# Optimization experiments

Hardware: AMD Instinct MI355X
Metric: run time of the kernel (lower is better)

## Reference

```python
import jax, jax.numpy as jnp
import numpy as np
import math

B, S, D, H, FF = 4, 1024, 1024, 16, 4096
DK = D // H
EPS = 1e-6


def _gelu(x):
    return 0.5 * x * (1 + jnp.tanh(math.sqrt(2 / math.pi) * (x + 0.044715 * x ** 3)))


def _layernorm(x, g, b):
    # torch LayerNorm clone: unbiased std, divide by (std + eps)
    mean = jnp.mean(x, axis=-1, keepdims=True)
    var = jnp.sum((x - mean) ** 2, axis=-1, keepdims=True) / (x.shape[-1] - 1)
    std = jnp.sqrt(var)
    return g * (x - mean) / (std + EPS) + b


def setup_inputs() -> dict:
    key = jax.random.key(0)
    ks = jax.random.split(key, 16)
    sc_d = 1.0 / math.sqrt(D)
    sc_ff = 1.0 / math.sqrt(FF)
    inp = {
        "query": jax.random.normal(ks[0], (B, S, D), jnp.float32),
        "key": jax.random.normal(ks[1], (B, S, D), jnp.float32),
        "value": jax.random.normal(ks[2], (B, S, D), jnp.float32),
        "mask": jnp.ones((B, S), jnp.int32),
        "Wq": jax.random.normal(ks[3], (D, D), jnp.float32) * sc_d,
        "bq": jnp.zeros((D,), jnp.float32),
        "Wk": jax.random.normal(ks[4], (D, D), jnp.float32) * sc_d,
        "bk": jnp.zeros((D,), jnp.float32),
        "Wv": jax.random.normal(ks[5], (D, D), jnp.float32) * sc_d,
        "bv": jnp.zeros((D,), jnp.float32),
        "Wo": jax.random.normal(ks[6], (D, D), jnp.float32) * sc_d,
        "bo": jnp.zeros((D,), jnp.float32),
        "W1": jax.random.normal(ks[7], (FF, D), jnp.float32) * sc_d,
        "b1": jnp.zeros((FF,), jnp.float32),
        "W2": jax.random.normal(ks[8], (D, FF), jnp.float32) * sc_ff,
        "b2": jnp.zeros((D,), jnp.float32),
        "g1": jnp.ones((D,), jnp.float32),
        "be1": jnp.zeros((D,), jnp.float32),
        "g2": jnp.ones((D,), jnp.float32),
        "be2": jnp.zeros((D,), jnp.float32),
    }
    return inp


def reference(query, key, value, mask, Wq, bq, Wk, bk, Wv, bv, Wo, bo,
              W1, b1, W2, b2, g1, be1, g2, be2):
    # self-attention: q = k = v = query (with_external=False)
    def proj(x, W, b):
        return (x @ W.T + b).reshape(B, S, H, DK).transpose(0, 2, 1, 3)  # [B,H,S,DK]

    q = proj(query, Wq, bq)
    k = proj(query, Wk, bk)
    v = proj(query, Wv, bv)
    scores = jnp.einsum("bhqd,bhkd->bhqk", q, k) / math.sqrt(DK)
    # 2D mask [B,S] broadcasts as [B,1,1,S] over key positions
    scores = jnp.where(mask[:, None, None, :] == 0, -1e9, scores)
    p = jax.nn.softmax(scores, axis=-1)
    attn = jnp.einsum("bhqk,bhkd->bhqd", p, v)
    attn = attn.transpose(0, 2, 1, 3).reshape(B, S, D)
    x = attn @ Wo.T + bo
    x = _layernorm(query + x, g1, be1)
    residual = x
    h1 = x @ W1.T + b1
    x2 = _gelu(h1 @ W2.T + b2)  # note: gelu applied AFTER fc2, per source
    return _layernorm(residual + x2, g2, be2)
```

## Files before the change

### kernel.cpp

```cpp
#include <hip/hip_runtime.h>
#include <hip/hip_bf16.h>
#include <math.h>

typedef __bf16 bf16;
typedef __bf16 bf16x8 __attribute__((ext_vector_type(8)));
typedef float floatx4 __attribute__((ext_vector_type(4)));

#define NT 4096
#define DMODEL 1024
#define NHEAD 16
#define DHEAD 64
#define FFDIM 4096

__device__ __forceinline__ void load_lds16(const void* g, void* l) {
    __builtin_amdgcn_global_load_lds(
        (const __attribute__((address_space(1))) void*)g,
        (__attribute__((address_space(3))) void*)l,
        16, 0, 0);
}

__device__ __forceinline__ unsigned short f2bf(float f) {
    bf16 h = (bf16)f;
    return __builtin_bit_cast(unsigned short, h);
}

__device__ __forceinline__ float gelu_f(float v) {
    return 0.5f * v * (1.0f + tanhf(0.7978845608028654f * (v + 0.044715f * v * v * v)));
}

__global__ __launch_bounds__(256) void cast_kernel(
    const float* __restrict__ q, const float* __restrict__ wq, const float* __restrict__ wk,
    const float* __restrict__ wv, const float* __restrict__ wo, const float* __restrict__ w1,
    const float* __restrict__ w2, const float* __restrict__ bq, const float* __restrict__ bk,
    const float* __restrict__ bv, bf16* __restrict__ xbf, bf16* __restrict__ wqkv,
    bf16* __restrict__ wob, bf16* __restrict__ w1b, bf16* __restrict__ w2b,
    float* __restrict__ bqkv)
{
    int gid = blockIdx.x * 256 + threadIdx.x;
    if (gid < 3072)
        bqkv[gid] = gid < 1024 ? bq[gid] : (gid < 2048 ? bk[gid - 1024] : bv[gid - 2048]);

    const float4* src;
    ushort4* dst;
    int off = gid;
    if (off < 1048576)                  { src = (const float4*)q;  dst = (ushort4*)xbf; }
    else if ((off -= 1048576) < 262144) { src = (const float4*)wq; dst = (ushort4*)wqkv; }
    else if ((off -= 262144) < 262144)  { src = (const float4*)wk; dst = (ushort4*)wqkv + 262144; }
    else if ((off -= 262144) < 262144)  { src = (const float4*)wv; dst = (ushort4*)wqkv + 524288; }
    else if ((off -= 262144) < 262144)  { src = (const float4*)wo; dst = (ushort4*)wob; }
    else if ((off -= 262144) < 1048576) { src = (const float4*)w1; dst = (ushort4*)w1b; }
    else { off -= 1048576;                src = (const float4*)w2; dst = (ushort4*)w2b; }

    float4 v = src[off];
    ushort4 u;
    u.x = f2bf(v.x); u.y = f2bf(v.y); u.z = f2bf(v.z); u.w = f2bf(v.w);
    dst[off] = u;
}

template <int EPI, int TN>
__global__ __launch_bounds__(256) void gemm_bt(
    const bf16* __restrict__ A, const bf16* __restrict__ Wt,
    const float* __restrict__ bias, const float* __restrict__ res,
    void* __restrict__ outp, int M, int N, int K)
{
    constexpr int NJ = TN / 32;
    __shared__ __align__(16) bf16 As[128 * 64];
    __shared__ __align__(16) bf16 Bs[TN * 64];

    const int t = threadIdx.x;
    const int lane = t & 63, wave = t >> 6;
    const int l15 = lane & 15, quad = lane >> 4;
    const int wm = wave & 1, wn = wave >> 1;
    const int m0 = blockIdx.x * 128, n0 = blockIdx.y * TN;

    floatx4 acc[4][NJ] = {};

    auto issue_loads = [&](int k0) {
        #pragma unroll
        for (int i = 0; i < 4; ++i) {
            int l = t + i * 256;
            int row = l >> 3, ch = (l & 7) ^ (row & 7);
            load_lds16(A + (size_t)(m0 + row) * K + k0 + ch * 8,
                       &As[(size_t)(i * 256 + wave * 64) * 8]);
        }
        #pragma unroll
        for (int i = 0; i < TN / 32; ++i) {
            int l = t + i * 256;
            int row = l >> 3, ch = (l & 7) ^ (row & 7);
            load_lds16(Wt + (size_t)(n0 + row) * K + k0 + ch * 8,
                       &Bs[(size_t)(i * 256 + wave * 64) * 8]);
        }
    };

    const int nk = K >> 6;
    issue_loads(0);

    for (int it = 0; it < nk; ++it) {
        __syncthreads();

        bf16x8 af[2][4], bfr[2][NJ];
        #pragma unroll
        for (int ks = 0; ks < 2; ++ks) {
            #pragma unroll
            for (int i = 0; i < 4; ++i) {
                int row = wm * 64 + i * 16 + l15;
                int pc = (ks * 4 + quad) ^ (row & 7);
                af[ks][i] = *(const bf16x8*)&As[row * 64 + pc * 8];
            }
            #pragma unroll
            for (int j = 0; j < NJ; ++j) {
                int row = wn * (TN / 2) + j * 16 + l15;
                int pc = (ks * 4 + quad) ^ (row & 7);
                bfr[ks][j] = *(const bf16x8*)&Bs[row * 64 + pc * 8];
            }
        }

        __syncthreads();

        if (it + 1 < nk) issue_loads((it + 1) << 6);

        #pragma unroll
        for (int ks = 0; ks < 2; ++ks)
            #pragma unroll
            for (int i = 0; i < 4; ++i)
                #pragma unroll
                for (int j = 0; j < NJ; ++j)
                    acc[i][j] = __builtin_amdgcn_mfma_f32_16x16x32_bf16(af[ks][i], bfr[ks][j], acc[i][j], 0, 0, 0);
    }

    const int mbase = m0 + wm * 64, nbase = n0 + wn * (TN / 2);
    #pragma unroll
    for (int i = 0; i < 4; ++i) {
        #pragma unroll
        for (int j = 0; j < NJ; ++j) {
            int col = nbase + j * 16 + l15;
            float bv = bias[col];
            #pragma unroll
            for (int r = 0; r < 4; ++r) {
                int row = mbase + i * 16 + quad * 4 + r;
                size_t idx = (size_t)row * N + col;
                float v = acc[i][j][r] + bv;
                if (EPI == 0) {
                    ((bf16*)outp)[idx] = (bf16)v;
                } else if (EPI == 1) {
                    ((float*)outp)[idx] = v + res[idx];
                } else {
                    ((float*)outp)[idx] = res[idx] + gelu_f(v);
                }
            }
        }
    }
}

__global__ __launch_bounds__(256) void transpose_v(const bf16* __restrict__ qkv,
                                                   bf16* __restrict__ vt)
{
    __shared__ bf16 tile[64 * 65];
    const int t = threadIdx.x;
    const int bh = blockIdx.y, bb = bh >> 4, h = bh & 15;
    const int s0 = blockIdx.x * 64;

    #pragma unroll
    for (int i = 0; i < 2; ++i) {
        int l = t + i * 256;
        int sl = l >> 3, c = (l & 7) * 8;
        bf16x8 v = *(const bf16x8*)(qkv + (size_t)(bb * 1024 + s0 + sl) * 3072 + 2048 + h * 64 + c);
        #pragma unroll
        for (int j = 0; j < 8; ++j) tile[sl * 65 + c + j] = v[j];
    }
    __syncthreads();
    #pragma unroll
    for (int i = 0; i < 2; ++i) {
        int l = t + i * 256;
        int dl = l >> 3, sc = (l & 7) * 8;
        bf16x8 v;
        #pragma unroll
        for (int j = 0; j < 8; ++j) v[j] = tile[(sc + j) * 65 + dl];
        *(bf16x8*)(vt + (size_t)(bh * 64 + dl) * 1024 + s0 + sc) = v;
    }
}

__global__ __launch_bounds__(256, 4) void flash_attn(
    const bf16* __restrict__ QKV, const bf16* __restrict__ VT,
    const int* __restrict__ mask, bf16* __restrict__ outp)
{
    __shared__ __align__(16) bf16 Ks[2][64 * 64];
    __shared__ __align__(16) bf16 VTs[2][64 * 64];

    const int t = threadIdx.x;
    const int lane = t & 63, wave = t >> 6;
    const int l15 = lane & 15, quad = lane >> 4;
    const int bh = blockIdx.x, bb = bh >> 4, h = bh & 15;
    const int q0 = blockIdx.y * 64;

    #pragma unroll
    for (int i = 0; i < 2; ++i) {
        int l = t + i * 256;
        int row = l >> 3, c = (l & 7) ^ (row & 7);
        load_lds16(QKV + (size_t)(bb * 1024 + q0 + row) * 3072 + h * 64 + c * 8,
                   &VTs[1][(size_t)(i * 256 + wave * 64) * 8]);
    }
    __syncthreads();

    bf16x8 aq[2];
    #pragma unroll
    for (int ks = 0; ks < 2; ++ks) {
        int row = wave * 16 + l15;
        int pc = (ks * 4 + quad) ^ (row & 7);
        aq[ks] = *(const bf16x8*)&VTs[1][row * 64 + pc * 8];
    }
    __syncthreads();

    auto stage_kv = [&](int buf, int kt) {
        #pragma unroll
        for (int i = 0; i < 2; ++i) {
            int l = t + i * 256;
            int row = l >> 3, c = (l & 7) ^ (row & 7);
            int gr = (row & 32) | ((row & 12) << 1) | ((row & 16) >> 2) | (row & 3);
            load_lds16(QKV + (size_t)(bb * 1024 + kt + gr) * 3072 + 1024 + h * 64 + c * 8,
                       &Ks[buf][(size_t)(i * 256 + wave * 64) * 8]);
            load_lds16(VT + (size_t)(bh * 64 + row) * 1024 + kt + c * 8,
                       &VTs[buf][(size_t)(i * 256 + wave * 64) * 8]);
        }
    };
    stage_kv(0, 0);

    floatx4 acc_o[4] = {};
    float m_st = -1e30f, l_st = 0.f;
    const float SC2 = 0.18033688011112042f;
    const float MB  = -1.442695e9f;
    const int* mrow = mask + bb * 1024;

    for (int kt = 0; kt < 1024; kt += 64) {
        const int buf = (kt >> 6) & 1;
        __syncthreads();
        if (kt + 64 < 1024) stage_kv(buf ^ 1, kt + 64);

        int mv = mrow[kt + lane];

        bf16x8 kf[2][4];
        #pragma unroll
        for (int ks = 0; ks < 2; ++ks)
            #pragma unroll
            for (int nt = 0; nt < 4; ++nt) {
                int row = nt * 16 + l15;
                int pc = (ks * 4 + quad) ^ (row & 7);
                kf[ks][nt] = *(const bf16x8*)&Ks[buf][row * 64 + pc * 8];
            }

        floatx4 s[4] = {};
        #pragma unroll
        for (int ks = 0; ks < 2; ++ks)
            #pragma unroll
            for (int nt = 0; nt < 4; ++nt)
                s[nt] = __builtin_amdgcn_mfma_f32_16x16x32_bf16(kf[ks][nt], aq[ks], s[nt], 0, 0, 0);

        bf16x8 vf[2][4];
        #pragma unroll
        for (int ks = 0; ks < 2; ++ks)
            #pragma unroll
            for (int nt2 = 0; nt2 < 4; ++nt2) {
                int row = nt2 * 16 + l15;
                int pc = (ks * 4 + quad) ^ (row & 7);
                vf[ks][nt2] = *(const bf16x8*)&VTs[buf][row * 64 + pc * 8];
            }

        float sv[4][4];
        if (__all(mv != 0)) {
            #pragma unroll
            for (int nt = 0; nt < 4; ++nt)
                #pragma unroll
                for (int r = 0; r < 4; ++r)
                    sv[nt][r] = s[nt][r] * SC2;
        } else {
            #pragma unroll
            for (int nt = 0; nt < 4; ++nt)
                #pragma unroll
                for (int r = 0; r < 4; ++r) {
                    int kg = ((nt >> 1) << 5) | (quad << 3) | ((nt & 1) << 2) | r;
                    int mk = __shfl(mv, kg, 64);
                    sv[nt][r] = fmaf(s[nt][r], SC2, mk ? 0.f : MB);
                }
        }

        float mx = sv[0][0];
        #pragma unroll
        for (int nt = 0; nt < 4; ++nt)
            #pragma unroll
            for (int r = 0; r < 4; ++r)
                mx = fmaxf(mx, sv[nt][r]);
        mx = fmaxf(mx, __shfl_xor(mx, 16, 64));
        mx = fmaxf(mx, __shfl_xor(mx, 32, 64));

        if (__any(mx > m_st + 12.0f)) {
            float mnew = fmaxf(m_st, mx);
            float al = __builtin_amdgcn_exp2f(m_st - mnew);
            m_st = mnew;
            l_st *= al;
            #pragma unroll
            for (int r = 0; r < 4; ++r) {
                float alr = __shfl(al, quad * 4 + r, 64);
                #pragma unroll
                for (int nt2 = 0; nt2 < 4; ++nt2) acc_o[nt2][r] *= alr;
            }
        }

        bf16x8 pa[2];
        float rs = 0.f;
        #pragma unroll
        for (int nt = 0; nt < 4; ++nt)
            #pragma unroll
            for (int r = 0; r < 4; ++r) {
                float p = __builtin_amdgcn_exp2f(sv[nt][r] - m_st);
                rs += p;
                pa[nt >> 1][(nt & 1) * 4 + r] = (bf16)p;
            }
        l_st += rs;

        #pragma unroll
        for (int ks = 0; ks < 2; ++ks)
            #pragma unroll
            for (int nt2 = 0; nt2 < 4; ++nt2)
                acc_o[nt2] = __builtin_amdgcn_mfma_f32_16x16x32_bf16(pa[ks], vf[ks][nt2], acc_o[nt2], 0, 0, 0);
    }

    float lt = l_st;
    lt += __shfl_xor(lt, 16, 64);
    lt += __shfl_xor(lt, 32, 64);
    #pragma unroll
    for (int r = 0; r < 4; ++r) {
        float lr = __shfl(lt, quad * 4 + r, 64);
        float linv = __builtin_amdgcn_rcpf(lr);
        int qrow = q0 + wave * 16 + quad * 4 + r;
        #pragma unroll
        for (int nt2 = 0; nt2 < 4; ++nt2) {
            int dd = nt2 * 16 + l15;
            outp[(size_t)(bb * 1024 + qrow) * 1024 + h * 64 + dd] = (bf16)(acc_o[nt2][r] * linv);
        }
    }
}

__global__ __launch_bounds__(256) void layernorm_k(
    const float* __restrict__ x, const float* __restrict__ g, const float* __restrict__ b,
    bf16* __restrict__ obf, float* __restrict__ of)
{
    const int row = blockIdx.x;
    float4 v = ((const float4*)(x + (size_t)row * 1024))[threadIdx.x];
    float s = v.x + v.y + v.z + v.w;
    float s2 = v.x * v.x + v.y * v.y + v.z * v.z + v.w * v.w;
    #pragma unroll
    for (int o = 32; o >= 1; o >>= 1) {
        s += __shfl_down(s, o, 64);
        s2 += __shfl_down(s2, o, 64);
    }
    __shared__ float red[8];
    if ((threadIdx.x & 63) == 0) {
        red[threadIdx.x >> 6] = s;
        red[4 + (threadIdx.x >> 6)] = s2;
    }
    __syncthreads();
    s = red[0] + red[1] + red[2] + red[3];
    s2 = red[4] + red[5] + red[6] + red[7];
    float mean = s * (1.f / 1024.f);
    float var = fmaxf(0.f, s2 - 1024.f * mean * mean) * (1.f / 1023.f);
    float inv = 1.f / (sqrtf(var) + 1e-6f);
    float4 gg = ((const float4*)g)[threadIdx.x];
    float4 bb = ((const float4*)b)[threadIdx.x];
    float4 o;
    o.x = gg.x * (v.x - mean) * inv + bb.x;
    o.y = gg.y * (v.y - mean) * inv + bb.y;
    o.z = gg.z * (v.z - mean) * inv + bb.z;
    o.w = gg.w * (v.w - mean) * inv + bb.w;
    if (of) ((float4*)(of + (size_t)row * 1024))[threadIdx.x] = o;
    if (obf) {
        ushort4 u;
        u.x = f2bf(o.x); u.y = f2bf(o.y); u.z = f2bf(o.z); u.w = f2bf(o.w);
        ((ushort4*)(obf + (size_t)row * 1024))[threadIdx.x] = u;
    }
}

constexpr size_t OFF_XBF   = 0;
constexpr size_t OFF_WQKV  = OFF_XBF + 8388608;
constexpr size_t OFF_BQKV  = OFF_WQKV + 6291456;
constexpr size_t OFF_WO    = OFF_BQKV + 16384;
constexpr size_t OFF_W1    = OFF_WO + 2097152;
constexpr size_t OFF_W2    = OFF_W1 + 8388608;
constexpr size_t OFF_QKV   = OFF_W2 + 8388608;
constexpr size_t OFF_VT    = OFF_QKV + 25165824;
constexpr size_t OFF_XRES1 = OFF_VT + 8388608;
constexpr size_t OFF_X1BF  = OFF_XRES1 + 16777216;
constexpr size_t OFF_X1F   = OFF_X1BF + 8388608;
constexpr size_t OFF_H1    = OFF_X1F + 16777216;

extern "C" void kernel_launch(void* const* d_in, const int* in_sizes, int n_in,
                              void* d_out, int out_size, void* d_ws, size_t ws_size,
                              hipStream_t stream)
{
    const float* query = (const float*)d_in[0];
    const int*   maskp = (const int*)d_in[3];
    const float* Wq = (const float*)d_in[4];
    const float* bq = (const float*)d_in[5];
    const float* Wk = (const float*)d_in[6];
    const float* bk = (const float*)d_in[7];
    const float* Wv = (const float*)d_in[8];
    const float* bv = (const float*)d_in[9];
    const float* Wo = (const float*)d_in[10];
    const float* bo = (const float*)d_in[11];
    const float* W1 = (const float*)d_in[12];
    const float* b1 = (const float*)d_in[13];
    const float* W2 = (const float*)d_in[14];
    const float* b2 = (const float*)d_in[15];
    const float* g1 = (const float*)d_in[16];
    const float* be1 = (const float*)d_in[17];
    const float* g2 = (const float*)d_in[18];
    const float* be2 = (const float*)d_in[19];

    char* ws = (char*)d_ws;
    bf16*  xbf   = (bf16*)(ws + OFF_XBF);
    bf16*  wqkv  = (bf16*)(ws + OFF_WQKV);
    float* bqkv  = (float*)(ws + OFF_BQKV);
    bf16*  wob   = (bf16*)(ws + OFF_WO);
    bf16*  w1b   = (bf16*)(ws + OFF_W1);
    bf16*  w2b   = (bf16*)(ws + OFF_W2);
    bf16*  qkv   = (bf16*)(ws + OFF_QKV);
    bf16*  vt    = (bf16*)(ws + OFF_VT);
    float* xres1 = (float*)(ws + OFF_XRES1);
    bf16*  x1bf  = (bf16*)(ws + OFF_X1BF);
    float* x1f   = (float*)(ws + OFF_X1F);
    bf16*  h1    = (bf16*)(ws + OFF_H1);
    bf16*  attn  = (bf16*)(ws + OFF_XBF);
    float* xres2 = (float*)(ws + OFF_QKV);
    float* outf  = (float*)d_out;

    cast_kernel<<<16384, 256, 0, stream>>>(query, Wq, Wk, Wv, Wo, W1, W2, bq, bk, bv,
                                           xbf, wqkv, wob, w1b, w2b, bqkv);
    gemm_bt<0, 128><<<dim3(32, 24), 256, 0, stream>>>(xbf, wqkv, bqkv, nullptr, qkv, NT, 3072, 1024);
    transpose_v<<<dim3(16, 64), 256, 0, stream>>>(qkv, vt);
    flash_attn<<<dim3(64, 16), 256, 0, stream>>>(qkv, vt, maskp, attn);
    gemm_bt<1, 64><<<dim3(32, 16), 256, 0, stream>>>(attn, wob, bo, query, xres1, NT, 1024, 1024);
    layernorm_k<<<4096, 256, 0, stream>>>(xres1, g1, be1, x1bf, x1f);
    gemm_bt<0, 128><<<dim3(32, 32), 256, 0, stream>>>(x1bf, w1b, b1, nullptr, h1, NT, 4096, 1024);
    gemm_bt<2, 64><<<dim3(32, 16), 256, 0, stream>>>(h1, w2b, b2, x1f, xres2, NT, 1024, 4096);
    layernorm_k<<<4096, 256, 0, stream>>>(xres2, g2, be2, nullptr, outf);
}
```

Measured before the change: 344.0 us.

## Split-K the N=1024 GEMMs with 128-wide tiles and fuse reduction into layernorm

The Wo and W2 projections now use 128-wide N tiles with a 2-way split-K. Each split writes raw fp32 partials into a scratch buffer that reuses the QKV region. The layernorm kernel now sums the two partials, adds bias and residual (plus GELU in the second use) before normalising, so the epilogue moves out of the GEMM. The split restores the block count lost to the wider tiles while keeping better operand reuse, at the cost of writing and reading an extra fp32 partial tensor.

```diff
diff --git a/kernel.cpp b/kernel.cpp
--- a/kernel.cpp
+++ b/kernel.cpp
@@ -57,7 +57,7 @@
     dst[off] = u;
 }
 
-template <int EPI, int TN>
+template <int EPI, int TN, int SPLITK = 1>
 __global__ __launch_bounds__(256) void gemm_bt(
     const bf16* __restrict__ A, const bf16* __restrict__ Wt,
     const float* __restrict__ bias, const float* __restrict__ res,
@@ -72,6 +72,9 @@
     const int l15 = lane & 15, quad = lane >> 4;
     const int wm = wave & 1, wn = wave >> 1;
     const int m0 = blockIdx.x * 128, n0 = blockIdx.y * TN;
+    const int kz = (SPLITK > 1) ? blockIdx.z : 0;
+    const int kspan = K / SPLITK;
+    const int kstart = kz * kspan;
 
     floatx4 acc[4][NJ] = {};
 
@@ -92,8 +95,8 @@
         }
     };
 
-    const int nk = K >> 6;
-    issue_loads(0);
+    const int nk = kspan >> 6;
+    issue_loads(kstart);
 
     for (int it = 0; it < nk; ++it) {
         __syncthreads();
@@ -117,7 +120,7 @@
 
         __syncthreads();
 
-        if (it + 1 < nk) issue_loads((it + 1) << 6);
+        if (it + 1 < nk) issue_loads(kstart + ((it + 1) << 6));
 
         #pragma unroll
         for (int ks = 0; ks < 2; ++ks)
@@ -129,12 +132,13 @@
     }
 
     const int mbase = m0 + wm * 64, nbase = n0 + wn * (TN / 2);
+    float* po = (float*)outp + (size_t)kz * ((size_t)M * N);
     #pragma unroll
     for (int i = 0; i < 4; ++i) {
         #pragma unroll
         for (int j = 0; j < NJ; ++j) {
             int col = nbase + j * 16 + l15;
-            float bv = bias[col];
+            float bv = (EPI == 3) ? 0.f : bias[col];
             #pragma unroll
             for (int r = 0; r < 4; ++r) {
                 int row = mbase + i * 16 + quad * 4 + r;
@@ -144,8 +148,10 @@
                     ((bf16*)outp)[idx] = (bf16)v;
                 } else if (EPI == 1) {
                     ((float*)outp)[idx] = v + res[idx];
+                } else if (EPI == 2) {
+                    ((float*)outp)[idx] = res[idx] + gelu_f(v);
                 } else {
-                    ((float*)outp)[idx] = res[idx] + gelu_f(v);
+                    po[idx] = v;
                 }
             }
         }
@@ -340,12 +346,31 @@
     }
 }
 
-__global__ __launch_bounds__(256) void layernorm_k(
-    const float* __restrict__ x, const float* __restrict__ g, const float* __restrict__ b,
-    bf16* __restrict__ obf, float* __restrict__ of)
+template <int MODE>
+__global__ __launch_bounds__(256) void ln_fuse(
+    const float* __restrict__ part, const float* __restrict__ res,
+    const float* __restrict__ bias, const float* __restrict__ g,
+    const float* __restrict__ b, bf16* __restrict__ obf, float* __restrict__ of)
 {
     const int row = blockIdx.x;
-    float4 v = ((const float4*)(x + (size_t)row * 1024))[threadIdx.x];
+    const size_t base = (size_t)row * 1024;
+    float4 p0 = ((const float4*)(part + base))[threadIdx.x];
+    float4 p1 = ((const float4*)(part + 4194304 + base))[threadIdx.x];
+    float4 rv = ((const float4*)(res + base))[threadIdx.x];
+    float4 bi = ((const float4*)bias)[threadIdx.x];
+    float4 v;
+    if (MODE == 0) {
+        v.x = rv.x + p0.x + p1.x + bi.x;
+        v.y = rv.y + p0.y + p1.y + bi.y;
+        v.z = rv.z + p0.z + p1.z + bi.z;
+        v.w = rv.w + p0.w + p1.w + bi.w;
+    } else {
+        v.x = rv.x + gelu_f(p0.x + p1.x + bi.x);
+        v.y = rv.y + gelu_f(p0.y + p1.y + bi.y);
+        v.z = rv.z + gelu_f(p0.z + p1.z + bi.z);
+        v.w = rv.w + gelu_f(p0.w + p1.w + bi.w);
+    }
+
     float s = v.x + v.y + v.z + v.w;
     float s2 = v.x * v.x + v.y * v.y + v.z * v.z + v.w * v.w;
     #pragma unroll
@@ -371,11 +396,11 @@
     o.y = gg.y * (v.y - mean) * inv + bb.y;
     o.z = gg.z * (v.z - mean) * inv + bb.z;
     o.w = gg.w * (v.w - mean) * inv + bb.w;
-    if (of) ((float4*)(of + (size_t)row * 1024))[threadIdx.x] = o;
+    if (of) ((float4*)(of + base))[threadIdx.x] = o;
     if (obf) {
         ushort4 u;
         u.x = f2bf(o.x); u.y = f2bf(o.y); u.z = f2bf(o.z); u.w = f2bf(o.w);
-        ((ushort4*)(obf + (size_t)row * 1024))[threadIdx.x] = u;
+        ((ushort4*)(obf + base))[threadIdx.x] = u;
     }
 }
 
@@ -387,8 +412,8 @@
 constexpr size_t OFF_W2    = OFF_W1 + 8388608;
 constexpr size_t OFF_QKV   = OFF_W2 + 8388608;
 constexpr size_t OFF_VT    = OFF_QKV + 25165824;
-constexpr size_t OFF_XRES1 = OFF_VT + 8388608;
-constexpr size_t OFF_X1BF  = OFF_XRES1 + 16777216;
+constexpr size_t OFF_PART  = OFF_QKV;
+constexpr size_t OFF_X1BF  = OFF_VT + 8388608;
 constexpr size_t OFF_X1F   = OFF_X1BF + 8388608;
 constexpr size_t OFF_H1    = OFF_X1F + 16777216;
 
@@ -424,12 +449,11 @@
     bf16*  w2b   = (bf16*)(ws + OFF_W2);
     bf16*  qkv   = (bf16*)(ws + OFF_QKV);
     bf16*  vt    = (bf16*)(ws + OFF_VT);
-    float* xres1 = (float*)(ws + OFF_XRES1);
+    float* part  = (float*)(ws + OFF_PART);
     bf16*  x1bf  = (bf16*)(ws + OFF_X1BF);
     float* x1f   = (float*)(ws + OFF_X1F);
     bf16*  h1    = (bf16*)(ws + OFF_H1);
     bf16*  attn  = (bf16*)(ws + OFF_XBF);
-    float* xres2 = (float*)(ws + OFF_QKV);
     float* outf  = (float*)d_out;
 
     cast_kernel<<<16384, 256, 0, stream>>>(query, Wq, Wk, Wv, Wo, W1, W2, bq, bk, bv,
@@ -437,9 +461,9 @@
     gemm_bt<0, 128><<<dim3(32, 24), 256, 0, stream>>>(xbf, wqkv, bqkv, nullptr, qkv, NT, 3072, 1024);
     transpose_v<<<dim3(16, 64), 256, 0, stream>>>(qkv, vt);
     flash_attn<<<dim3(64, 16), 256, 0, stream>>>(qkv, vt, maskp, attn);
-    gemm_bt<1, 64><<<dim3(32, 16), 256, 0, stream>>>(attn, wob, bo, query, xres1, NT, 1024, 1024);
-    layernorm_k<<<4096, 256, 0, stream>>>(xres1, g1, be1, x1bf, x1f);
+    gemm_bt<3, 128, 2><<<dim3(32, 8, 2), 256, 0, stream>>>(attn, wob, nullptr, nullptr, part, NT, 1024, 1024);
+    ln_fuse<0><<<4096, 256, 0, stream>>>(part, query, bo, g1, be1, x1bf, x1f);
     gemm_bt<0, 128><<<dim3(32, 32), 256, 0, stream>>>(x1bf, w1b, b1, nullptr, h1, NT, 4096, 1024);
-    gemm_bt<2, 64><<<dim3(32, 16), 256, 0, stream>>>(h1, w2b, b2, x1f, xres2, NT, 1024, 4096);
-    layernorm_k<<<4096, 256, 0, stream>>>(xres2, g2, be2, nullptr, outf);
-}
+    gemm_bt<3, 128, 2><<<dim3(32, 8, 2), 256, 0, stream>>>(h1, w2b, nullptr, nullptr, part, NT, 1024, 4096);
+    ln_fuse<1><<<4096, 256, 0, stream>>>(part, x1f, b2, g2, be2, nullptr, outf);
+}
```

Measured after the change: 331.2 us. 3.7% less time.
